# Kernel tuning notes

Hardware: AMD Instinct MI355X
Metric: run time of the kernel (lower is better)

Reference implementation:

```python
import jax, jax.numpy as jnp
import numpy as np

B, H, W = 32, 32, 32
C_CNN, C_EFF, HID = 512, 1280, 512


def conv1x1(x, w, b):
    # x: [B, Cin, H, W], w: [Cout, Cin], b: [Cout]
    return jnp.einsum('bchw,oc->bohw', x, w) + b[None, :, None, None]


def setup_inputs() -> dict:
    key = jax.random.key(0)
    ks = jax.random.split(key, 12)
    s = 0.02  # small init scale keeps softmax logits well-conditioned
    return {
        'cnn_features': jax.random.normal(ks[0], (B, C_CNN, H, W), jnp.float32),
        'efficient_features': jax.random.normal(ks[1], (B, C_EFF, H, W), jnp.float32),
        'W_cnn': jax.random.normal(ks[2], (HID, C_CNN), jnp.float32) * s,
        'b_cnn': jnp.zeros((HID,), jnp.float32),
        'W_eff': jax.random.normal(ks[3], (HID, C_EFF), jnp.float32) * s,
        'b_eff': jnp.zeros((HID,), jnp.float32),
        'W_q': jax.random.normal(ks[4], (HID, HID), jnp.float32) * s,
        'b_q': jnp.zeros((HID,), jnp.float32),
        'W_k': jax.random.normal(ks[5], (HID, HID), jnp.float32) * s,
        'b_k': jnp.zeros((HID,), jnp.float32),
        'W_v': jax.random.normal(ks[6], (HID, HID), jnp.float32) * s,
        'b_v': jnp.zeros((HID,), jnp.float32),
        'gamma': jnp.asarray([0.1], jnp.float32),
    }


def reference(cnn_features, efficient_features, W_cnn, b_cnn, W_eff, b_eff,
              W_q, b_q, W_k, b_k, W_v, b_v, gamma):
    cnn_proj = conv1x1(cnn_features, W_cnn, b_cnn)          # [B, HID, H, W]
    eff_proj = conv1x1(efficient_features, W_eff, b_eff)    # [B, HID, H, W]
    b, c, h, w = cnn_proj.shape
    n = h * w
    # 1x1 conv QKV projections then flatten spatial dims into tokens
    q = conv1x1(cnn_proj, W_q, b_q).reshape(b, c, n).transpose(0, 2, 1)  # [B, N, C]
    k = conv1x1(eff_proj, W_k, b_k).reshape(b, c, n)                     # [B, C, N]
    v = conv1x1(eff_proj, W_v, b_v).reshape(b, c, n).transpose(0, 2, 1)  # [B, N, C]
    attn = jax.nn.softmax(jnp.einsum('bnc,bcm->bnm', q, k), axis=-1)     # [B, N, N] (unscaled, as in source)
    out = jnp.einsum('bnm,bmc->bnc', attn, v)                            # [B, N, C]
    out = out.transpose(0, 2, 1).reshape(b, c, h, w)
    return gamma[0] * out + cnn_proj
```

## Files before the change

### kernel.cpp

```cpp
#include <hip/hip_runtime.h>
#include <hip/hip_bf16.h>
#include <cstdint>


typedef __hip_bfloat16 bf16;
typedef __bf16 bf16x8 __attribute__((ext_vector_type(8)));
typedef float f32x4 __attribute__((ext_vector_type(4)));

#define NB   32
#define NTOK 1024
#define NHID 512
#define CEFF 1280
#define WSZ  (NHID*NHID)

struct W4 { const float* s[4]; };
__global__ __launch_bounds__(256) void convert_w4_kernel(W4 w, bf16* __restrict__ dst) {
    int i = blockIdx.x * 256 + threadIdx.x;
    int sel = i >> 18, off = i & (WSZ - 1);
    dst[i] = __float2bfloat16(w.s[sel][off]);
}

__global__ __launch_bounds__(256) void transpose_to_bf16_kernel(const float* __restrict__ in,
                                                                bf16* __restrict__ out,
                                                                int C, int N) {
    __shared__ float tile[32][33];
    const int n0 = blockIdx.x * 32, c0 = blockIdx.y * 32, b = blockIdx.z;
    in  += (size_t)b * C * N;
    out += (size_t)b * N * C;
    const int tx = threadIdx.x, ty = threadIdx.y;
    #pragma unroll
    for (int i = ty; i < 32; i += 8)
        tile[i][tx] = in[(size_t)(c0 + i) * N + n0 + tx];
    __syncthreads();
    #pragma unroll
    for (int i = ty; i < 32; i += 8)
        out[(size_t)(n0 + i) * C + c0 + tx] = __float2bfloat16(tile[tx][i]);
}

__global__ __launch_bounds__(256) void bias_fuse_kernel(
    const float* __restrict__ Wq, const float* __restrict__ Wk, const float* __restrict__ Wv,
    const float* __restrict__ bc, const float* __restrict__ be,
    const float* __restrict__ bq, const float* __restrict__ bk, const float* __restrict__ bv,
    float* __restrict__ bqc, float* __restrict__ bkv) {
    const int r = blockIdx.x, t = threadIdx.x;
    const float* Wrow; const float* vin; float badd; float* dst;
    if (r < 512)       { Wrow = Wq + (size_t)r * 512;          vin = bc; badd = bq[r];        dst = bqc + r; }
    else if (r < 1024) { Wrow = Wk + (size_t)(r - 512) * 512;  vin = be; badd = bk[r - 512];  dst = bkv + (r - 512); }
    else               { Wrow = Wv + (size_t)(r - 1024) * 512; vin = be; badd = bv[r - 1024]; dst = bkv + (r - 512); }
    float s = Wrow[t] * vin[t] + Wrow[t + 256] * vin[t + 256];
    #pragma unroll
    for (int off = 32; off >= 1; off >>= 1) s += __shfl_xor(s, off, 64);
    __shared__ float red[4];
    if ((t & 63) == 0) red[t >> 6] = s;
    __syncthreads();
    if (t == 0) dst[0] = red[0] + red[1] + red[2] + red[3] + badd;
}

__global__ __launch_bounds__(256) void gemm_bt_kernel(
    const bf16* __restrict__ A, long long aStride, int lda,
    const bf16* __restrict__ Bt, long long bStride, int ldb,
    int K, int swiz,
    const float* __restrict__ bias,
    float* __restrict__ outF, long long fStride, int ldf,
    const bf16* __restrict__ residH, const float* __restrict__ gammaPtr,
    const float* __restrict__ rsumIn,
    float* __restrict__ rsumOut,
    bf16* __restrict__ outHt, long long htStride, int ldht, int htMax,
    bf16* __restrict__ outHn, long long hnStride, int ldhn, int hnBase, int doExp)
{
    __shared__ __bf16 lA[128 * 32];
    __shared__ __bf16 lB[128 * 32];
    __shared__ float lrs[128];

    const int tid  = threadIdx.x;
    const int wave = tid >> 6;
    const int lane = tid & 63;

    int bx, by, bz;
    if (swiz) { bx = (int)blockIdx.y & 7; by = (int)blockIdx.y >> 3; bz = (int)blockIdx.z * 8 + (int)blockIdx.x; }
    else      { bx = (int)blockIdx.x;     by = (int)blockIdx.y;      bz = (int)blockIdx.z; }
    const int m0 = by * 128;
    const int n0 = bx * 128;

    const bf16* Ab = A  + (size_t)bz * aStride;
    const bf16* Bb = Bt + (size_t)bz * bStride;

    const int wm = wave >> 1, wn = wave & 1;
    const int lrow = lane & 15, quad = lane >> 4;

    f32x4 acc[4][4];
    #pragma unroll
    for (int i = 0; i < 4; i++)
        #pragma unroll
        for (int j = 0; j < 4; j++)
            acc[i][j] = (f32x4){0.f, 0.f, 0.f, 0.f};

    const int rowl = lane >> 2;
    const int qsw  = (lane & 3) ^ ((lane >> 3) & 3);
    const bf16* gA0 = Ab + (size_t)(m0 +      wave * 16 + rowl) * lda + qsw * 8;
    const bf16* gA1 = Ab + (size_t)(m0 + 64 + wave * 16 + rowl) * lda + qsw * 8;
    const bf16* gB0 = Bb + (size_t)(n0 +      wave * 16 + rowl) * ldb + qsw * 8;
    const bf16* gB1 = Bb + (size_t)(n0 + 64 + wave * 16 + rowl) * ldb + qsw * 8;
    __bf16* lA0 = &lA[(wave * 64) * 8];
    __bf16* lA1 = &lA[(256 + wave * 64) * 8];
    __bf16* lB0 = &lB[(wave * 64) * 8];
    __bf16* lB1 = &lB[(256 + wave * 64) * 8];

    const int sw = quad ^ ((lrow >> 1) & 3);
    int aoff[4], boff[4];
    #pragma unroll
    for (int mt = 0; mt < 4; mt++) aoff[mt] = ((wm * 4 + mt) * 64 + lrow * 4 + sw) * 8;
    #pragma unroll
    for (int nt = 0; nt < 4; nt++) boff[nt] = ((wn * 4 + nt) * 64 + lrow * 4 + sw) * 8;

    for (int k0 = 0; k0 < K; k0 += 32) {
        __builtin_amdgcn_global_load_lds((const __attribute__((address_space(1))) void*)(gA0 + k0),
                                         (__attribute__((address_space(3))) void*)lA0, 16, 0, 0);
        __builtin_amdgcn_global_load_lds((const __attribute__((address_space(1))) void*)(gA1 + k0),
                                         (__attribute__((address_space(3))) void*)lA1, 16, 0, 0);
        __builtin_amdgcn_global_load_lds((const __attribute__((address_space(1))) void*)(gB0 + k0),
                                         (__attribute__((address_space(3))) void*)lB0, 16, 0, 0);
        __builtin_amdgcn_global_load_lds((const __attribute__((address_space(1))) void*)(gB1 + k0),
                                         (__attribute__((address_space(3))) void*)lB1, 16, 0, 0);
        __syncthreads();

        bf16x8 af[4], bfr[4];
        #pragma unroll
        for (int mt = 0; mt < 4; mt++) af[mt]  = *(const bf16x8*)&lA[aoff[mt]];
        #pragma unroll
        for (int nt = 0; nt < 4; nt++) bfr[nt] = *(const bf16x8*)&lB[boff[nt]];
        #pragma unroll
        for (int mt = 0; mt < 4; mt++)
            #pragma unroll
            for (int nt = 0; nt < 4; nt++)
                acc[mt][nt] = __builtin_amdgcn_mfma_f32_16x16x32_bf16(af[mt], bfr[nt], acc[mt][nt], 0, 0, 0);
        __syncthreads();
    }

    const float gscale = gammaPtr ? gammaPtr[0] : 1.0f;
    float rs[4][4];
    if (rsumOut)
        #pragma unroll
        for (int mt = 0; mt < 4; mt++)
            #pragma unroll
            for (int r = 0; r < 4; r++) rs[mt][r] = 0.f;

    #pragma unroll
    for (int mt = 0; mt < 4; mt++) {
        const int mbase = m0 + wm * 64 + mt * 16 + quad * 4;
        float bv[4];
        #pragma unroll
        for (int r = 0; r < 4; r++) bv[r] = bias ? bias[mbase + r] : 0.f;
        #pragma unroll
        for (int nt = 0; nt < 4; nt++) {
            const int n = n0 + wn * 64 + nt * 16 + lrow;
            float v[4];
            #pragma unroll
            for (int r = 0; r < 4; r++) {
                v[r] = acc[mt][nt][r] + bv[r];
                if (doExp) v[r] = __expf(v[r]);
                if (rsumOut) rs[mt][r] += v[r];
            }
            if (outF) {
                float* p = outF + (size_t)bz * fStride;
                const bf16* rp = residH + (size_t)bz * fStride;
                const float rinv = rsumIn ? 1.0f / rsumIn[(size_t)bz * NTOK + n] : 1.0f;
                #pragma unroll
                for (int r = 0; r < 4; r++) {
                    size_t idx = (size_t)(mbase + r) * ldf + n;
                    p[idx] = gscale * v[r] * rinv + __bfloat162float(rp[idx]);
                }
            }
            if (outHt && mbase < htMax) {
                union { bf16 h[4]; unsigned long long u; } pk;
                #pragma unroll
                for (int r = 0; r < 4; r++) pk.h[r] = __float2bfloat16(v[r]);
                *(unsigned long long*)&outHt[(size_t)bz * htStride + (size_t)n * ldht + mbase] = pk.u;
            }
            if (outHn && mbase >= hnBase) {
                bf16* p = outHn + (size_t)bz * hnStride;
                #pragma unroll
                for (int r = 0; r < 4; r++)
                    p[(size_t)(mbase - hnBase + r) * ldhn + n] = __float2bfloat16(v[r]);
            }
        }
    }

    if (rsumOut) {
        #pragma unroll
        for (int mt = 0; mt < 4; mt++)
            #pragma unroll
            for (int r = 0; r < 4; r++) {
                float s = rs[mt][r];
                s += __shfl_xor(s, 1, 64);
                s += __shfl_xor(s, 2, 64);
                s += __shfl_xor(s, 4, 64);
                s += __shfl_xor(s, 8, 64);
                rs[mt][r] = s;
            }
        if (tid < 128) lrs[tid] = 0.f;
        __syncthreads();
        if (lrow == 0) {
            #pragma unroll
            for (int mt = 0; mt < 4; mt++)
                #pragma unroll
                for (int r = 0; r < 4; r++)
                    atomicAdd(&lrs[wm * 64 + mt * 16 + quad * 4 + r], rs[mt][r]);
        }
        __syncthreads();
        if (tid < 128) atomicAdd(&rsumOut[(size_t)bz * NTOK + m0 + tid], lrs[tid]);
    }
}

extern "C" void kernel_launch(void* const* d_in, const int* in_sizes, int n_in,
                              void* d_out, int out_size, void* d_ws, size_t ws_size,
                              hipStream_t stream) {
    const float* x_cnn = (const float*)d_in[0];
    const float* x_eff = (const float*)d_in[1];
    const float* W_cnn = (const float*)d_in[2];
    const float* b_cnn = (const float*)d_in[3];
    const float* W_eff = (const float*)d_in[4];
    const float* b_eff = (const float*)d_in[5];
    const float* W_q   = (const float*)d_in[6];
    const float* b_q   = (const float*)d_in[7];
    const float* W_k   = (const float*)d_in[8];
    const float* b_k   = (const float*)d_in[9];
    const float* W_v   = (const float*)d_in[10];
    const float* b_v   = (const float*)d_in[11];
    const float* gamma = (const float*)d_in[12];
    float* out = (float*)d_out;

    uint8_t* ws = (uint8_t*)d_ws;
    size_t off = 0;
    auto alloc = [&](size_t bytes) -> uint8_t* {
        uint8_t* p = ws + off;
        off = (off + bytes + 255) & ~(size_t)255;
        return p;
    };

    bf16* Wall  = (bf16*)alloc((size_t)4 * WSZ * 2);
    bf16* Wc_h  = Wall;
    bf16* Wq_h  = Wall + WSZ;
    bf16* Wkv_h = Wall + 2 * (size_t)WSZ;
    bf16* Wct   = (bf16*)alloc((size_t)NHID * NHID * 2);
    bf16* Wet   = (bf16*)alloc((size_t)CEFF * NHID * 2);
    bf16* Wqc   = (bf16*)alloc((size_t)NHID * NHID * 2);
    bf16* Wkve  = (bf16*)alloc((size_t)1024 * CEFF * 2);
    float* bqc  = (float*)alloc(NHID * 4);
    float* bkv  = (float*)alloc(1024 * 4);
    float* rowSum = (float*)alloc((size_t)NB * NTOK * 4);
    bf16* Xc_t  = (bf16*)alloc((size_t)NB * NTOK * NHID * 2);
    bf16* Xe_t  = (bf16*)alloc((size_t)NB * NTOK * CEFF * 2);
    bf16* resid = (bf16*)alloc((size_t)NB * NHID * NTOK * 2);
    bf16* q_t   = (bf16*)alloc((size_t)NB * NTOK * NHID * 2);
    bf16* k_t   = (bf16*)alloc((size_t)NB * NTOK * NHID * 2);
    bf16* v_nt  = (bf16*)alloc((size_t)NB * NHID * NTOK * 2);
    bf16* P     = Xe_t;

    {
        W4 w; w.s[0] = W_cnn; w.s[1] = W_q; w.s[2] = W_k; w.s[3] = W_v;
        convert_w4_kernel<<<4 * WSZ / 256, 256, 0, stream>>>(w, Wall);
    }
    transpose_to_bf16_kernel<<<dim3(NHID / 32, NHID / 32, 1), dim3(32, 8), 0, stream>>>(W_cnn, Wct, NHID, NHID);
    transpose_to_bf16_kernel<<<dim3(CEFF / 32, NHID / 32, 1), dim3(32, 8), 0, stream>>>(W_eff, Wet, NHID, CEFF);

    transpose_to_bf16_kernel<<<dim3(NTOK / 32, NHID / 32, NB), dim3(32, 8), 0, stream>>>(x_cnn, Xc_t, NHID, NTOK);
    transpose_to_bf16_kernel<<<dim3(NTOK / 32, CEFF / 32, NB), dim3(32, 8), 0, stream>>>(x_eff, Xe_t, CEFF, NTOK);

    bias_fuse_kernel<<<1536, 256, 0, stream>>>(W_q, W_k, W_v, b_cnn, b_eff, b_q, b_k, b_v, bqc, bkv);

    hipMemsetAsync(rowSum, 0, (size_t)NB * NTOK * 4, stream);

    auto gemm = [&](dim3 grid, int swiz,
                    const bf16* A, long long aS, int lda,
                    const bf16* Bt, long long bS, int ldb, int K,
                    const float* bias,
                    float* oF, long long fS, int ldf, const bf16* rH, const float* gp,
                    const float* rIn, float* rOut,
                    bf16* oHt, long long htS, int ldht, int htMax,
                    bf16* oHn, long long hnS, int ldhn, int hnBase, int doExp) {
        gemm_bt_kernel<<<grid, 256, 0, stream>>>(A, aS, lda, Bt, bS, ldb, K, swiz, bias,
                                                 oF, fS, ldf, rH, gp, rIn, rOut,
                                                 oHt, htS, ldht, htMax, oHn, hnS, ldhn, hnBase, doExp);
    };

    const long long sNC = (long long)NTOK * NHID;
    const long long sCN = (long long)NHID * NTOK;
    const long long sNE = (long long)NTOK * CEFF;
    const long long sPP = (long long)NTOK * NTOK;

    gemm(dim3(4, 4, 1), 0, Wq_h, 0, NHID, Wct, 0, NHID, NHID, nullptr,
         nullptr, 0, 0, nullptr, nullptr, nullptr, nullptr,
         nullptr, 0, 0, 0, Wqc, 0, NHID, 0, 0);
    gemm(dim3(10, 8, 1), 0, Wkv_h, 0, NHID, Wet, 0, NHID, NHID, nullptr,
         nullptr, 0, 0, nullptr, nullptr, nullptr, nullptr,
         nullptr, 0, 0, 0, Wkve, 0, CEFF, 0, 0);

    gemm(dim3(8, 32, 4), 1, Wc_h, 0, NHID, Xc_t, sNC, NHID, NHID, b_cnn,
         nullptr, 0, 0, nullptr, nullptr, nullptr, nullptr,
         nullptr, 0, 0, 0, resid, sCN, NTOK, 0, 0);
    gemm(dim3(8, 32, 4), 1, Wqc, 0, NHID, Xc_t, sNC, NHID, NHID, bqc,
         nullptr, 0, 0, nullptr, nullptr, nullptr, nullptr,
         q_t, sNC, NHID, 1 << 30, nullptr, 0, 0, 0, 0);
    gemm(dim3(8, 64, 4), 1, Wkve, 0, CEFF, Xe_t, sNE, CEFF, CEFF, bkv,
         nullptr, 0, 0, nullptr, nullptr, nullptr, nullptr,
         k_t, sNC, NHID, NHID,
         v_nt, sCN, NTOK, NHID, 0);
    gemm(dim3(8, 64, 4), 1, q_t, sNC, NHID, k_t, sNC, NHID, NHID, nullptr,
         nullptr, 0, 0, nullptr, nullptr, nullptr, rowSum,
         nullptr, 0, 0, 0, P, sPP, NTOK, 0, 1);
    gemm(dim3(8, 32, 4), 1, v_nt, sCN, NTOK, P, sPP, NTOK, NTOK, nullptr,
         out, sCN, NTOK, resid, gamma, rowSum, nullptr,
         nullptr, 0, 0, 0, nullptr, 0, 0, 0, 0);
}
```

Baseline: 789.4 us.

## Double-buffer GEMM LDS tiles and merge resid/q projections into one GEMM

The GEMM main loop now uses two LDS buffers. The next K-slice is issued with global_load_lds while the current one is computed, and the full barrier pair is replaced by waitcnt plus s_barrier. This is meant to hide global load latency behind the MFMA work. Separately, the cnn projection and the fused q projection are stacked into one 1024-row weight matrix with a stacked bias, so Xc_t is read once in a single launch instead of two. The cost is double the LDS per block, which may lower occupancy, plus extra device-to-device copies.

```diff
diff --git a/kernel.cpp b/kernel.cpp
--- a/kernel.cpp
+++ b/kernel.cpp
@@ -68,8 +68,8 @@
     bf16* __restrict__ outHt, long long htStride, int ldht, int htMax,
     bf16* __restrict__ outHn, long long hnStride, int ldhn, int hnBase, int doExp)
 {
-    __shared__ __bf16 lA[128 * 32];
-    __shared__ __bf16 lB[128 * 32];
+    __shared__ __bf16 lA[2][128 * 32];
+    __shared__ __bf16 lB[2][128 * 32];
     __shared__ float lrs[128];
 
     const int tid  = threadIdx.x;
@@ -101,10 +101,8 @@
     const bf16* gA1 = Ab + (size_t)(m0 + 64 + wave * 16 + rowl) * lda + qsw * 8;
     const bf16* gB0 = Bb + (size_t)(n0 +      wave * 16 + rowl) * ldb + qsw * 8;
     const bf16* gB1 = Bb + (size_t)(n0 + 64 + wave * 16 + rowl) * ldb + qsw * 8;
-    __bf16* lA0 = &lA[(wave * 64) * 8];
-    __bf16* lA1 = &lA[(256 + wave * 64) * 8];
-    __bf16* lB0 = &lB[(wave * 64) * 8];
-    __bf16* lB1 = &lB[(256 + wave * 64) * 8];
+    const int dst0 = (wave * 64) * 8;
+    const int dst1 = (256 + wave * 64) * 8;
 
     const int sw = quad ^ ((lrow >> 1) & 3);
     int aoff[4], boff[4];
@@ -113,29 +111,48 @@
     #pragma unroll
     for (int nt = 0; nt < 4; nt++) boff[nt] = ((wn * 4 + nt) * 64 + lrow * 4 + sw) * 8;
 
-    for (int k0 = 0; k0 < K; k0 += 32) {
+    auto stage = [&](int k0, int b) {
         __builtin_amdgcn_global_load_lds((const __attribute__((address_space(1))) void*)(gA0 + k0),
-                                         (__attribute__((address_space(3))) void*)lA0, 16, 0, 0);
+                                         (__attribute__((address_space(3))) void*)(&lA[b][dst0]), 16, 0, 0);
         __builtin_amdgcn_global_load_lds((const __attribute__((address_space(1))) void*)(gA1 + k0),
-                                         (__attribute__((address_space(3))) void*)lA1, 16, 0, 0);
+                                         (__attribute__((address_space(3))) void*)(&lA[b][dst1]), 16, 0, 0);
         __builtin_amdgcn_global_load_lds((const __attribute__((address_space(1))) void*)(gB0 + k0),
-                                         (__attribute__((address_space(3))) void*)lB0, 16, 0, 0);
+                                         (__attribute__((address_space(3))) void*)(&lB[b][dst0]), 16, 0, 0);
         __builtin_amdgcn_global_load_lds((const __attribute__((address_space(1))) void*)(gB1 + k0),
-                                         (__attribute__((address_space(3))) void*)lB1, 16, 0, 0);
-        __syncthreads();
-
+                                         (__attribute__((address_space(3))) void*)(&lB[b][dst1]), 16, 0, 0);
+    };
+
+    auto compute = [&](int b) {
+        const __bf16* __restrict__ pA = lA[b];
+        const __bf16* __restrict__ pB = lB[b];
         bf16x8 af[4], bfr[4];
         #pragma unroll
-        for (int mt = 0; mt < 4; mt++) af[mt]  = *(const bf16x8*)&lA[aoff[mt]];
-        #pragma unroll
-        for (int nt = 0; nt < 4; nt++) bfr[nt] = *(const bf16x8*)&lB[boff[nt]];
+        for (int mt = 0; mt < 4; mt++) af[mt]  = *(const bf16x8*)&pA[aoff[mt]];
+        #pragma unroll
+        for (int nt = 0; nt < 4; nt++) bfr[nt] = *(const bf16x8*)&pB[boff[nt]];
         #pragma unroll
         for (int mt = 0; mt < 4; mt++)
             #pragma unroll
             for (int nt = 0; nt < 4; nt++)
                 acc[mt][nt] = __builtin_amdgcn_mfma_f32_16x16x32_bf16(af[mt], bfr[nt], acc[mt][nt], 0, 0, 0);
-        __syncthreads();
+    };
+
+    stage(0, 0);
+    int cur = 0;
+    for (int k0 = 32; k0 < K; k0 += 32) {
+        stage(k0, cur ^ 1);
+        asm volatile("s_waitcnt vmcnt(4)" ::: "memory");
+        __builtin_amdgcn_s_barrier();
+        asm volatile("" ::: "memory");
+        compute(cur);
+        asm volatile("s_waitcnt lgkmcnt(0)" ::: "memory");
+        __builtin_amdgcn_s_barrier();
+        cur ^= 1;
     }
+    asm volatile("s_waitcnt vmcnt(0)" ::: "memory");
+    __builtin_amdgcn_s_barrier();
+    asm volatile("" ::: "memory");
+    compute(cur);
 
     const float gscale = gammaPtr ? gammaPtr[0] : 1.0f;
     float rs[4][4];
@@ -244,9 +261,9 @@
     bf16* Wkv_h = Wall + 2 * (size_t)WSZ;
     bf16* Wct   = (bf16*)alloc((size_t)NHID * NHID * 2);
     bf16* Wet   = (bf16*)alloc((size_t)CEFF * NHID * 2);
-    bf16* Wqc   = (bf16*)alloc((size_t)NHID * NHID * 2);
+    bf16* Wstack= (bf16*)alloc((size_t)1024 * NHID * 2);
     bf16* Wkve  = (bf16*)alloc((size_t)1024 * CEFF * 2);
-    float* bqc  = (float*)alloc(NHID * 4);
+    float* bstack = (float*)alloc(1024 * 4);
     float* bkv  = (float*)alloc(1024 * 4);
     float* rowSum = (float*)alloc((size_t)NB * NTOK * 4);
     bf16* Xc_t  = (bf16*)alloc((size_t)NB * NTOK * NHID * 2);
@@ -267,7 +284,10 @@
     transpose_to_bf16_kernel<<<dim3(NTOK / 32, NHID / 32, NB), dim3(32, 8), 0, stream>>>(x_cnn, Xc_t, NHID, NTOK);
     transpose_to_bf16_kernel<<<dim3(NTOK / 32, CEFF / 32, NB), dim3(32, 8), 0, stream>>>(x_eff, Xe_t, CEFF, NTOK);
 
-    bias_fuse_kernel<<<1536, 256, 0, stream>>>(W_q, W_k, W_v, b_cnn, b_eff, b_q, b_k, b_v, bqc, bkv);
+    bias_fuse_kernel<<<1536, 256, 0, stream>>>(W_q, W_k, W_v, b_cnn, b_eff, b_q, b_k, b_v, bstack, bkv);
+    hipMemcpyAsync(Wstack + (size_t)NHID * NHID, Wc_h, (size_t)NHID * NHID * 2,
+                   hipMemcpyDeviceToDevice, stream);
+    hipMemcpyAsync(bstack + NHID, b_cnn, NHID * 4, hipMemcpyDeviceToDevice, stream);
 
     hipMemsetAsync(rowSum, 0, (size_t)NB * NTOK * 4, stream);
 
@@ -291,17 +311,15 @@
 
     gemm(dim3(4, 4, 1), 0, Wq_h, 0, NHID, Wct, 0, NHID, NHID, nullptr,
          nullptr, 0, 0, nullptr, nullptr, nullptr, nullptr,
-         nullptr, 0, 0, 0, Wqc, 0, NHID, 0, 0);
+         nullptr, 0, 0, 0, Wstack, 0, NHID, 0, 0);
     gemm(dim3(10, 8, 1), 0, Wkv_h, 0, NHID, Wet, 0, NHID, NHID, nullptr,
          nullptr, 0, 0, nullptr, nullptr, nullptr, nullptr,
          nullptr, 0, 0, 0, Wkve, 0, CEFF, 0, 0);
 
-    gemm(dim3(8, 32, 4), 1, Wc_h, 0, NHID, Xc_t, sNC, NHID, NHID, b_cnn,
+    gemm(dim3(8, 64, 4), 1, Wstack, 0, NHID, Xc_t, sNC, NHID, NHID, bstack,
          nullptr, 0, 0, nullptr, nullptr, nullptr, nullptr,
-         nullptr, 0, 0, 0, resid, sCN, NTOK, 0, 0);
-    gemm(dim3(8, 32, 4), 1, Wqc, 0, NHID, Xc_t, sNC, NHID, NHID, bqc,
-         nullptr, 0, 0, nullptr, nullptr, nullptr, nullptr,
-         q_t, sNC, NHID, 1 << 30, nullptr, 0, 0, 0, 0);
+         q_t, sNC, NHID, NHID,
+         resid, sCN, NTOK, NHID, 0);
     gemm(dim3(8, 64, 4), 1, Wkve, 0, CEFF, Xe_t, sNE, CEFF, CEFF, bkv,
          nullptr, 0, 0, nullptr, nullptr, nullptr, nullptr,
          k_t, sNC, NHID, NHID,
```

Measured after the change: 726.7 us. 1.09x faster.
